# Kernel tuning notes

Hardware: AMD Instinct MI355X
Metric: run time of the kernel (lower is better)

## Reference

```python
import jax, jax.numpy as jnp
import numpy as np

N_NODES = 100000
N_EDGES = 1200000
IN_DIM = 64
OUT_DIM = 64
LN_EPS = 1e-5


def setup_inputs() -> dict:
    key = jax.random.key(0)
    k_x, k_e, k_w, k_b, k_g, k_beta = jax.random.split(key, 6)
    x = jax.random.normal(k_x, (N_NODES, IN_DIM), dtype=jnp.float32)
    edge_index = jax.random.randint(k_e, (2, N_EDGES), 0, N_NODES, dtype=jnp.int64)
    # nn.Linear(in_dim*2, out_dim): weight [out, 2*in], bias [out]
    lim = 1.0 / np.sqrt(2 * IN_DIM)
    W = jax.random.uniform(k_w, (OUT_DIM, 2 * IN_DIM), minval=-lim, maxval=lim, dtype=jnp.float32)
    b = jax.random.uniform(k_b, (OUT_DIM,), minval=-lim, maxval=lim, dtype=jnp.float32)
    gamma = jnp.ones((OUT_DIM,), dtype=jnp.float32)
    beta = jnp.zeros((OUT_DIM,), dtype=jnp.float32)
    return {"x": x, "W": W, "b": b, "gamma": gamma, "beta": beta, "edge_index": edge_index}


def reference(x, W, b, gamma, beta, edge_index):
    i = edge_index[0]  # destination nodes (aggregation target)
    j = edge_index[1]  # source nodes (neighbor features)
    n = x.shape[0]
    # mean aggregation: scatter-add gathered neighbor feats, divide by degree
    agg = jax.ops.segment_sum(x[j], i, num_segments=n)  # [N, in_dim]
    deg = jax.ops.segment_sum(jnp.ones(i.shape, x.dtype), i, num_segments=n)
    agg = agg / jnp.maximum(deg, 1.0)[:, None]
    # concat + linear + relu
    h = jnp.concatenate([x, agg], axis=-1) @ W.T + b  # [N, out_dim]
    h = jax.nn.relu(h)
    # layernorm (dropout p=0 is identity in eval)
    mu = jnp.mean(h, axis=-1, keepdims=True)
    var = jnp.var(h, axis=-1, keepdims=True)
    return (h - mu) / jnp.sqrt(var + LN_EPS) * gamma + beta
```

## Files before the change

kernel.cpp:

```cpp
#include <hip/hip_runtime.h>
#include <hip/hip_bf16.h>

#define N_NODES 100000
#define N_EDGES 1200000
#define LN_EPS 1e-5f
#define CAP 40
#define NBIN 782
#define NREP 8
#define BCAPR 288
#define EPB 4096
#define P1_BLOCKS 293
#define CONV_BLOCKS 507
#define NSTRIDE 42
#define NBLK2 1563
#define QENC (127.0f / 5.2f)
#define QDEC (5.2f / 127.0f)

typedef __attribute__((ext_vector_type(8))) short short8;
typedef __attribute__((ext_vector_type(8))) unsigned short us8;
typedef __attribute__((ext_vector_type(4))) float float4v;
typedef __attribute__((ext_vector_type(2))) int   ivec2;

__device__ __forceinline__ short bfb(float v) {
    __hip_bfloat16 h = __float2bfloat16(v);
    short s; __builtin_memcpy(&s, &h, 2); return s;
}
__device__ __forceinline__ int q8(float v) {
    return (int)rintf(fminf(fmaxf(v * QENC, -127.0f), 127.0f));
}

__global__ __launch_bounds__(256) void k_bin3(
    const float* __restrict__ x, unsigned short* __restrict__ xb,
    char* __restrict__ xq,
    const float* __restrict__ W, unsigned short* __restrict__ Wb,
    const int* __restrict__ ei, int* __restrict__ btail,
    int* __restrict__ binbuf)
{
    const int tid = threadIdx.x;

    if (blockIdx.x >= P1_BLOCKS) {
        if (blockIdx.x == P1_BLOCKS) {
            if (tid < 8) {
                short8 z = {0, 0, 0, 0, 0, 0, 0, 0};
                *(short8*)(xb + (size_t)N_NODES * 64 + tid * 8) = z;
                *(ivec2*)(xq + (size_t)N_NODES * 64 + tid * 8) = (ivec2){0, 0};
            }
#pragma unroll
            for (int it = 0; it < 32; ++it) {
                int i = it * 256 + tid;
                Wb[i] = (unsigned short)bfb(W[i]);
            }
        }
        for (int i = (blockIdx.x - P1_BLOCKS) * 256 + tid; i < N_NODES * 8;
             i += CONV_BLOCKS * 256) {
            float4v f0 = *(const float4v*)(x + 8 * i);
            float4v f1 = *(const float4v*)(x + 8 * i + 4);
            short8 p;
            p[0] = bfb(f0.x); p[1] = bfb(f0.y); p[2] = bfb(f0.z); p[3] = bfb(f0.w);
            p[4] = bfb(f1.x); p[5] = bfb(f1.y); p[6] = bfb(f1.z); p[7] = bfb(f1.w);
            *(short8*)(xb + 8 * i) = p;
            int w0 = (q8(f0.x) & 255) | ((q8(f0.y) & 255) << 8) |
                     ((q8(f0.z) & 255) << 16) | ((q8(f0.w) & 255) << 24);
            int w1 = (q8(f1.x) & 255) | ((q8(f1.y) & 255) << 8) |
                     ((q8(f1.z) & 255) << 16) | ((q8(f1.w) & 255) << 24);
            *(ivec2*)(xq + 8 * (size_t)i) = (ivec2){w0, w1};
        }
        return;
    }

    __shared__ int   bcnt[NBIN];
    __shared__ int   bbase[NBIN];
    __shared__ int   bgbase[NBIN];
    __shared__ int   bfill[NBIN];
    __shared__ int   scanbuf[256];
    __shared__ ivec2 stage[EPB];

    const int rep = blockIdx.x & (NREP - 1);

    for (int i = tid; i < NBIN; i += 256) { bcnt[i] = 0; bfill[i] = 0; }
    __syncthreads();

    const int ebase = blockIdx.x * EPB;
    int d[16], s[16];
#pragma unroll
    for (int u = 0; u < 16; ++u) {
        int e = ebase + u * 256 + tid;
        bool v = (e < N_EDGES);
        d[u] = v ? ei[e] : -1;
        s[u] = v ? ei[N_EDGES + e] : 0;
        if (v) atomicAdd(&bcnt[d[u] >> 7], 1);
    }
    __syncthreads();

    int v4[4], tsum = 0;
#pragma unroll
    for (int k = 0; k < 4; ++k) {
        int b = 4 * tid + k;
        v4[k] = (b < NBIN) ? bcnt[b] : 0;
        tsum += v4[k];
    }
    scanbuf[tid] = tsum;
    __syncthreads();
    for (int off = 1; off < 256; off <<= 1) {
        int t = (tid >= off) ? scanbuf[tid - off] : 0;
        __syncthreads();
        scanbuf[tid] += t;
        __syncthreads();
    }
    int run = scanbuf[tid] - tsum;
#pragma unroll
    for (int k = 0; k < 4; ++k) {
        int b = 4 * tid + k;
        if (b < NBIN) bbase[b] = run;
        run += v4[k];
    }
    const int tot = scanbuf[255];

    for (int b = tid; b < NBIN; b += 256) {
        int c = bcnt[b];
        bgbase[b] = c ? atomicAdd(&btail[rep * NBIN + b], c) : 0;
    }
    __syncthreads();

#pragma unroll
    for (int u = 0; u < 16; ++u) {
        if (d[u] >= 0) {
            int b = d[u] >> 7;
            int p = bbase[b] + atomicAdd(&bfill[b], 1);
            stage[p] = (ivec2){d[u], s[u]};
        }
    }
    __syncthreads();

    for (int i = tid; i < tot; i += 256) {
        ivec2 e = stage[i];
        int b = e.x >> 7;
        int pos = bgbase[b] + (i - bbase[b]);
        if (pos < BCAPR)
            binbuf[((size_t)rep * NBIN + b) * BCAPR + pos] = ((e.x & 127) << 17) | e.y;
    }
}

__global__ __launch_bounds__(256, 4) void node_fused(
    const unsigned short* __restrict__ xb, const char* __restrict__ xq,
    const unsigned short* __restrict__ Wb,
    const int* __restrict__ btail, const int* __restrict__ binbuf,
    const float* __restrict__ bias,
    const float* __restrict__ gamma, const float* __restrict__ beta,
    float* __restrict__ out)
{
    __shared__ short Wl[64 * 136];
    __shared__ int   nlist[64 * NSTRIDE];
    __shared__ int   lcnt[64];

    const int tid = threadIdx.x;
    const int bin  = blockIdx.x >> 1;
    const int half = blockIdx.x & 1;
    const int nodebase = blockIdx.x * 64;

#pragma unroll
    for (int it = 0; it < 4; ++it) {
        int i = it * 256 + tid;
        int row = i >> 4, c8 = i & 15;
        *(short8*)&Wl[row * 136 + c8 * 8] = *(const short8*)(Wb + row * 128 + c8 * 8);
    }
    if (tid < 64) lcnt[tid] = 0;
    __syncthreads();

#pragma unroll
    for (int rep = 0; rep < NREP; ++rep) {
        const int nb = min(btail[rep * NBIN + bin], BCAPR);
        const int* bp = binbuf + ((size_t)rep * NBIN + bin) * BCAPR;
        for (int i = tid; i < nb; i += 256) {
            int pk = bp[i];
            int nl = (pk >> 17) - (half << 6);
            if ((unsigned)nl < 64u) {
                int slot = atomicAdd(&lcnt[nl], 1);
                if (slot < CAP) nlist[nl * NSTRIDE + slot] = pk & 0x1FFFF;
            }
        }
    }
    __syncthreads();

    const int wid  = tid >> 6;
    const int lane = tid & 63;
    const int g    = lane >> 4;
    const int c    = lane & 15;
    const int ch   = c & 7;
    const int pr   = c >> 3;
    const int nbase = nodebase + wid * 16;
    if (nbase >= N_NODES) return;

    int dfull[4], dgs[4];
#pragma unroll
    for (int r = 0; r < 4; ++r) {
        dfull[r] = lcnt[wid * 16 + r * 4 + g];
        dgs[r]   = min(dfull[r], CAP);
    }
    int aai[4][8];
#pragma unroll
    for (int r = 0; r < 4; ++r)
#pragma unroll
        for (int k = 0; k < 8; ++k) aai[r][k] = 0;

    const int dmax = max(max(dgs[0], dgs[1]), max(dgs[2], dgs[3]));
    for (int t = 0; t < dmax; t += 16) {
        ivec2 vv[32];
#pragma unroll
        for (int u = 0; u < 8; ++u)
#pragma unroll
            for (int r = 0; r < 4; ++r) {
                int idx = t + 2 * u + pr;
                int wl  = nlist[(wid * 16 + r * 4 + g) * NSTRIDE + idx];
                int j   = (idx < dgs[r]) ? wl : N_NODES;
                vv[u * 4 + r] = *(const ivec2*)(xq + (size_t)j * 64 + ch * 8);
            }
#pragma unroll
        for (int u = 0; u < 8; ++u)
#pragma unroll
            for (int r = 0; r < 4; ++r) {
                int w0 = vv[u * 4 + r].x, w1 = vv[u * 4 + r].y;
                aai[r][0] += (w0 << 24) >> 24;
                aai[r][1] += (w0 << 16) >> 24;
                aai[r][2] += (w0 << 8)  >> 24;
                aai[r][3] +=  w0 >> 24;
                aai[r][4] += (w1 << 24) >> 24;
                aai[r][5] += (w1 << 16) >> 24;
                aai[r][6] += (w1 << 8)  >> 24;
                aai[r][7] +=  w1 >> 24;
            }
    }

    const unsigned short* xrow = xb + (size_t)(nbase + c) * 64 + g * 8;
    short8 A0 = *(const short8*)(xrow);
    short8 A1 = *(const short8*)(xrow + 32);

#pragma unroll
    for (int r = 0; r < 4; ++r)
#pragma unroll
        for (int k = 0; k < 8; ++k) aai[r][k] += __shfl_xor(aai[r][k], 8);

    short* aL = (short*)&nlist[wid * 16 * NSTRIDE];
#pragma unroll
    for (int r = 0; r < 4; ++r) {
        float rd = QDEC / fmaxf((float)dfull[r], 1.0f);
        int m = r * 4 + g;
        short8 p;
#pragma unroll
        for (int k = 0; k < 8; ++k) p[k] = bfb((float)aai[r][k] * rd);
        if (pr == 0)
            *(short8*)(aL + m * 72 + ch * 8) = p;
    }
    short8 A2 = *(const short8*)(aL + c * 72 + g * 8);
    short8 A3 = *(const short8*)(aL + c * 72 + 32 + g * 8);

    float bs_[4], gm_[4], bt_[4];
#pragma unroll
    for (int ct = 0; ct < 4; ++ct) {
        bs_[ct] = bias[ct * 16 + c];
        gm_[ct] = gamma[ct * 16 + c];
        bt_[ct] = beta[ct * 16 + c];
    }

    float4v acc[4];
#pragma unroll
    for (int ct = 0; ct < 4; ++ct) {
        float bb = bs_[ct];
        acc[ct] = (float4v){bb, bb, bb, bb};
    }
#pragma unroll
    for (int ks = 0; ks < 4; ++ks) {
        short8 Af = (ks == 0) ? A0 : (ks == 1) ? A1 : (ks == 2) ? A2 : A3;
#pragma unroll
        for (int ct = 0; ct < 4; ++ct) {
            short8 Bf = *(const short8*)(Wl + (ct * 16 + c) * 136 + ks * 32 + g * 8);
            acc[ct] = __builtin_amdgcn_mfma_f32_16x16x32_bf16(Af, Bf, acc[ct], 0, 0, 0);
        }
    }

    float s_[4] = {0, 0, 0, 0}, q_[4] = {0, 0, 0, 0};
#pragma unroll
    for (int ct = 0; ct < 4; ++ct)
#pragma unroll
        for (int r = 0; r < 4; ++r) {
            float h = fmaxf(acc[ct][r], 0.0f);
            acc[ct][r] = h;
            s_[r] += h;
            q_[r] += h * h;
        }
#pragma unroll
    for (int off = 1; off <= 8; off <<= 1)
#pragma unroll
        for (int r = 0; r < 4; ++r) {
            s_[r] += __shfl_xor(s_[r], off);
            q_[r] += __shfl_xor(q_[r], off);
        }
#pragma unroll
    for (int r = 0; r < 4; ++r) {
        float mu = s_[r] * (1.0f / 64.0f);
        float var = q_[r] * (1.0f / 64.0f) - mu * mu;
        float is = rsqrtf(var + LN_EPS);
        int node = nbase + g * 4 + r;
        if (node < N_NODES) {
#pragma unroll
            for (int ct = 0; ct < 4; ++ct) {
                out[node * 64 + ct * 16 + c] =
                    (acc[ct][r] - mu) * is * gm_[ct] + bt_[ct];
            }
        }
    }
}

extern "C" void kernel_launch(void* const* d_in, const int* in_sizes, int n_in,
                              void* d_out, int out_size, void* d_ws, size_t ws_size,
                              hipStream_t stream) {
    const float* x     = (const float*)d_in[0];
    const float* W     = (const float*)d_in[1];
    const float* b     = (const float*)d_in[2];
    const float* gamma = (const float*)d_in[3];
    const float* beta  = (const float*)d_in[4];
    const int*   ei    = (const int*)d_in[5];
    float* out = (float*)d_out;

    int* btail = (int*)d_ws;
    int* binbuf = (int*)((char*)d_ws + 32768);
    unsigned short* xb = (unsigned short*)(binbuf + (size_t)NREP * NBIN * BCAPR);
    unsigned short* Wb = xb + (size_t)(N_NODES + 1) * 64;
    char* xq = (char*)(Wb + 8192);

    (void)hipMemsetAsync(btail, 0, NREP * NBIN * sizeof(int), stream);

    k_bin3<<<P1_BLOCKS + CONV_BLOCKS, 256, 0, stream>>>(x, xb, xq, W, Wb, ei, btail, binbuf);
    node_fused<<<NBLK2, 256, 0, stream>>>(xb, xq, Wb, btail, binbuf, b, gamma, beta, out);
}
```

Measured before the change: 134.6 us.

## Aggregate neighbor features via LDS atomics per 128-node bin

Replaces the per-node neighbor-list build followed by register accumulation with an edge-parallel scheme. Each block processes a whole 128-node bin, gathers the quantized source rows and adds them into a shared int accumulator with LDS atomics, then runs the MFMA and layernorm epilogue on two 16-node groups per wave. The goal is to remove the degree cap and the load imbalance from padding to the max degree across nodes, and to halve the block count. The cost is many LDS atomic adds (eight per edge per channel group), W read from global instead of LDS, and a larger shared-memory footprint.

```diff
diff --git a/kernel.cpp b/kernel.cpp
--- a/kernel.cpp
+++ b/kernel.cpp
@@ -4,20 +4,16 @@
 #define N_NODES 100000
 #define N_EDGES 1200000
 #define LN_EPS 1e-5f
-#define CAP 40
 #define NBIN 782
 #define NREP 8
 #define BCAPR 288
 #define EPB 4096
 #define P1_BLOCKS 293
 #define CONV_BLOCKS 507
-#define NSTRIDE 42
-#define NBLK2 1563
 #define QENC (127.0f / 5.2f)
 #define QDEC (5.2f / 127.0f)
 
 typedef __attribute__((ext_vector_type(8))) short short8;
-typedef __attribute__((ext_vector_type(8))) unsigned short us8;
 typedef __attribute__((ext_vector_type(4))) float float4v;
 typedef __attribute__((ext_vector_type(2))) int   ivec2;
 
@@ -149,35 +145,59 @@
     const float* __restrict__ gamma, const float* __restrict__ beta,
     float* __restrict__ out)
 {
-    __shared__ short Wl[64 * 136];
-    __shared__ int   nlist[64 * NSTRIDE];
-    __shared__ int   lcnt[64];
+    __shared__ int agg[129][66];
+    __shared__ int deg[132];
 
     const int tid = threadIdx.x;
-    const int bin  = blockIdx.x >> 1;
-    const int half = blockIdx.x & 1;
-    const int nodebase = blockIdx.x * 64;
-
-#pragma unroll
-    for (int it = 0; it < 4; ++it) {
-        int i = it * 256 + tid;
-        int row = i >> 4, c8 = i & 15;
-        *(short8*)&Wl[row * 136 + c8 * 8] = *(const short8*)(Wb + row * 128 + c8 * 8);
-    }
-    if (tid < 64) lcnt[tid] = 0;
-    __syncthreads();
-
-#pragma unroll
-    for (int rep = 0; rep < NREP; ++rep) {
-        const int nb = min(btail[rep * NBIN + bin], BCAPR);
-        const int* bp = binbuf + ((size_t)rep * NBIN + bin) * BCAPR;
-        for (int i = tid; i < nb; i += 256) {
-            int pk = bp[i];
-            int nl = (pk >> 17) - (half << 6);
-            if ((unsigned)nl < 64u) {
-                int slot = atomicAdd(&lcnt[nl], 1);
-                if (slot < CAP) nlist[nl * NSTRIDE + slot] = pk & 0x1FFFF;
-            }
+    const int bin = blockIdx.x;
+
+    for (int i = tid; i < 129 * 66; i += 256) ((int*)agg)[i] = 0;
+    if (tid < 132) deg[tid] = 0;
+    __syncthreads();
+
+    int cum[NREP + 1];
+    cum[0] = 0;
+#pragma unroll
+    for (int r2 = 0; r2 < NREP; ++r2)
+        cum[r2 + 1] = cum[r2] + min(btail[r2 * NBIN + bin], BCAPR);
+    const int etot = cum[NREP];
+
+    const int eo = tid >> 3;
+    const int ch = tid & 7;
+
+    for (int base = 0; base < etot; base += 512) {
+        int pk[16];
+#pragma unroll
+        for (int u = 0; u < 16; ++u) {
+            int v = base + u * 32 + eo;
+            int rp = 0;
+#pragma unroll
+            for (int k2 = 1; k2 < NREP; ++k2) rp += (v >= cum[k2]);
+            int idx = v - cum[rp];
+            pk[u] = (v < etot)
+                  ? binbuf[((size_t)rp * NBIN + bin) * BCAPR + idx]
+                  : ((128 << 17) | N_NODES);
+        }
+        ivec2 vv[16];
+#pragma unroll
+        for (int u = 0; u < 16; ++u) {
+            int j = pk[u] & 0x1FFFF;
+            vv[u] = *(const ivec2*)(xq + (size_t)j * 64 + ch * 8);
+        }
+#pragma unroll
+        for (int u = 0; u < 16; ++u) {
+            int nl = pk[u] >> 17;
+            int w0 = vv[u].x, w1 = vv[u].y;
+            int* ap = &agg[nl][ch * 8];
+            atomicAdd(ap + 0, (w0 << 24) >> 24);
+            atomicAdd(ap + 1, (w0 << 16) >> 24);
+            atomicAdd(ap + 2, (w0 << 8)  >> 24);
+            atomicAdd(ap + 3,  w0 >> 24);
+            atomicAdd(ap + 4, (w1 << 24) >> 24);
+            atomicAdd(ap + 5, (w1 << 16) >> 24);
+            atomicAdd(ap + 6, (w1 << 8)  >> 24);
+            atomicAdd(ap + 7,  w1 >> 24);
+            if (ch == 0) atomicAdd(&deg[nl], 1);
         }
     }
     __syncthreads();
@@ -186,73 +206,6 @@
     const int lane = tid & 63;
     const int g    = lane >> 4;
     const int c    = lane & 15;
-    const int ch   = c & 7;
-    const int pr   = c >> 3;
-    const int nbase = nodebase + wid * 16;
-    if (nbase >= N_NODES) return;
-
-    int dfull[4], dgs[4];
-#pragma unroll
-    for (int r = 0; r < 4; ++r) {
-        dfull[r] = lcnt[wid * 16 + r * 4 + g];
-        dgs[r]   = min(dfull[r], CAP);
-    }
-    int aai[4][8];
-#pragma unroll
-    for (int r = 0; r < 4; ++r)
-#pragma unroll
-        for (int k = 0; k < 8; ++k) aai[r][k] = 0;
-
-    const int dmax = max(max(dgs[0], dgs[1]), max(dgs[2], dgs[3]));
-    for (int t = 0; t < dmax; t += 16) {
-        ivec2 vv[32];
-#pragma unroll
-        for (int u = 0; u < 8; ++u)
-#pragma unroll
-            for (int r = 0; r < 4; ++r) {
-                int idx = t + 2 * u + pr;
-                int wl  = nlist[(wid * 16 + r * 4 + g) * NSTRIDE + idx];
-                int j   = (idx < dgs[r]) ? wl : N_NODES;
-                vv[u * 4 + r] = *(const ivec2*)(xq + (size_t)j * 64 + ch * 8);
-            }
-#pragma unroll
-        for (int u = 0; u < 8; ++u)
-#pragma unroll
-            for (int r = 0; r < 4; ++r) {
-                int w0 = vv[u * 4 + r].x, w1 = vv[u * 4 + r].y;
-                aai[r][0] += (w0 << 24) >> 24;
-                aai[r][1] += (w0 << 16) >> 24;
-                aai[r][2] += (w0 << 8)  >> 24;
-                aai[r][3] +=  w0 >> 24;
-                aai[r][4] += (w1 << 24) >> 24;
-                aai[r][5] += (w1 << 16) >> 24;
-                aai[r][6] += (w1 << 8)  >> 24;
-                aai[r][7] +=  w1 >> 24;
-            }
-    }
-
-    const unsigned short* xrow = xb + (size_t)(nbase + c) * 64 + g * 8;
-    short8 A0 = *(const short8*)(xrow);
-    short8 A1 = *(const short8*)(xrow + 32);
-
-#pragma unroll
-    for (int r = 0; r < 4; ++r)
-#pragma unroll
-        for (int k = 0; k < 8; ++k) aai[r][k] += __shfl_xor(aai[r][k], 8);
-
-    short* aL = (short*)&nlist[wid * 16 * NSTRIDE];
-#pragma unroll
-    for (int r = 0; r < 4; ++r) {
-        float rd = QDEC / fmaxf((float)dfull[r], 1.0f);
-        int m = r * 4 + g;
-        short8 p;
-#pragma unroll
-        for (int k = 0; k < 8; ++k) p[k] = bfb((float)aai[r][k] * rd);
-        if (pr == 0)
-            *(short8*)(aL + m * 72 + ch * 8) = p;
-    }
-    short8 A2 = *(const short8*)(aL + c * 72 + g * 8);
-    short8 A3 = *(const short8*)(aL + c * 72 + 32 + g * 8);
 
     float bs_[4], gm_[4], bt_[4];
 #pragma unroll
@@ -262,50 +215,68 @@
         bt_[ct] = beta[ct * 16 + c];
     }
 
-    float4v acc[4];
-#pragma unroll
-    for (int ct = 0; ct < 4; ++ct) {
-        float bb = bs_[ct];
-        acc[ct] = (float4v){bb, bb, bb, bb};
-    }
-#pragma unroll
-    for (int ks = 0; ks < 4; ++ks) {
-        short8 Af = (ks == 0) ? A0 : (ks == 1) ? A1 : (ks == 2) ? A2 : A3;
+    for (int gi = 0; gi < 2; ++gi) {
+        const int nbase = bin * 128 + wid * 32 + gi * 16;
+        if (nbase >= N_NODES) break;
+
+        const unsigned short* xrow = xb + (size_t)(nbase + c) * 64 + g * 8;
+        short8 A0 = *(const short8*)(xrow);
+        short8 A1 = *(const short8*)(xrow + 32);
+
+        const int nloc = wid * 32 + gi * 16 + c;
+        const float rd = QDEC / fmaxf((float)deg[nloc], 1.0f);
+        short8 A2, A3;
+#pragma unroll
+        for (int k2 = 0; k2 < 8; ++k2) {
+            A2[k2] = bfb((float)agg[nloc][g * 8 + k2] * rd);
+            A3[k2] = bfb((float)agg[nloc][32 + g * 8 + k2] * rd);
+        }
+
+        float4v acc[4];
 #pragma unroll
         for (int ct = 0; ct < 4; ++ct) {
-            short8 Bf = *(const short8*)(Wl + (ct * 16 + c) * 136 + ks * 32 + g * 8);
-            acc[ct] = __builtin_amdgcn_mfma_f32_16x16x32_bf16(Af, Bf, acc[ct], 0, 0, 0);
-        }
-    }
-
-    float s_[4] = {0, 0, 0, 0}, q_[4] = {0, 0, 0, 0};
-#pragma unroll
-    for (int ct = 0; ct < 4; ++ct)
+            float bb = bs_[ct];
+            acc[ct] = (float4v){bb, bb, bb, bb};
+        }
+#pragma unroll
+        for (int ks = 0; ks < 4; ++ks) {
+            short8 Af = (ks == 0) ? A0 : (ks == 1) ? A1 : (ks == 2) ? A2 : A3;
+#pragma unroll
+            for (int ct = 0; ct < 4; ++ct) {
+                short8 Bf = *(const short8*)(Wb + (ct * 16 + c) * 128 + ks * 32 + g * 8);
+                acc[ct] = __builtin_amdgcn_mfma_f32_16x16x32_bf16(Af, Bf, acc[ct], 0, 0, 0);
+            }
+        }
+
+        float s_[4] = {0, 0, 0, 0}, q_[4] = {0, 0, 0, 0};
+#pragma unroll
+        for (int ct = 0; ct < 4; ++ct)
+#pragma unroll
+            for (int r = 0; r < 4; ++r) {
+                float h = fmaxf(acc[ct][r], 0.0f);
+                acc[ct][r] = h;
+                s_[r] += h;
+                q_[r] += h * h;
+            }
+#pragma unroll
+        for (int off = 1; off <= 8; off <<= 1)
+#pragma unroll
+            for (int r = 0; r < 4; ++r) {
+                s_[r] += __shfl_xor(s_[r], off);
+                q_[r] += __shfl_xor(q_[r], off);
+            }
 #pragma unroll
         for (int r = 0; r < 4; ++r) {
-            float h = fmaxf(acc[ct][r], 0.0f);
-            acc[ct][r] = h;
-            s_[r] += h;
-            q_[r] += h * h;
-        }
-#pragma unroll
-    for (int off = 1; off <= 8; off <<= 1)
-#pragma unroll
-        for (int r = 0; r < 4; ++r) {
-            s_[r] += __shfl_xor(s_[r], off);
-            q_[r] += __shfl_xor(q_[r], off);
-        }
-#pragma unroll
-    for (int r = 0; r < 4; ++r) {
-        float mu = s_[r] * (1.0f / 64.0f);
-        float var = q_[r] * (1.0f / 64.0f) - mu * mu;
-        float is = rsqrtf(var + LN_EPS);
-        int node = nbase + g * 4 + r;
-        if (node < N_NODES) {
-#pragma unroll
-            for (int ct = 0; ct < 4; ++ct) {
-                out[node * 64 + ct * 16 + c] =
-                    (acc[ct][r] - mu) * is * gm_[ct] + bt_[ct];
+            float mu = s_[r] * (1.0f / 64.0f);
+            float var = q_[r] * (1.0f / 64.0f) - mu * mu;
+            float is = rsqrtf(var + LN_EPS);
+            int node = nbase + g * 4 + r;
+            if (node < N_NODES) {
+#pragma unroll
+                for (int ct = 0; ct < 4; ++ct) {
+                    out[node * 64 + ct * 16 + c] =
+                        (acc[ct][r] - mu) * is * gm_[ct] + bt_[ct];
+                }
             }
         }
     }
@@ -331,5 +302,5 @@
     (void)hipMemsetAsync(btail, 0, NREP * NBIN * sizeof(int), stream);
 
     k_bin3<<<P1_BLOCKS + CONV_BLOCKS, 256, 0, stream>>>(x, xb, xq, W, Wb, ei, btail, binbuf);
-    node_fused<<<NBLK2, 256, 0, stream>>>(xb, xq, Wb, btail, binbuf, b, gamma, beta, out);
-}
+    node_fused<<<NBIN, 256, 0, stream>>>(xb, xq, Wb, btail, binbuf, b, gamma, beta, out);
+}
```

New measurement: 157.2 us. 16.8% more time.

## Drop bf16 copy of x, read fp32 directly; double edges per binning block

Applied to the files above, without the earlier changes.

Removes the intermediate bf16 copy of x: node_fused now reads fp32 rows of x directly and converts them to bf16 in registers. This drops one full write of x and the matching read of the bf16 buffer. The binning kernel now handles 8192 edges per block with half as many blocks, re-reading edge indices in the second pass instead of holding them in registers. Its LDS stage array is split into a packed int plus a 16-bit bin id. In exchange, node_fused reads twice as many bytes for its own rows, and the binning phase has fewer blocks and reads ei twice.

```diff
diff --git a/kernel.cpp b/kernel.cpp
--- a/kernel.cpp
+++ b/kernel.cpp
@@ -8,8 +8,8 @@
 #define NBIN 782
 #define NREP 8
 #define BCAPR 288
-#define EPB 4096
-#define P1_BLOCKS 293
+#define EPB 8192
+#define P1_BLOCKS 147
 #define CONV_BLOCKS 507
 #define NSTRIDE 42
 #define NBLK2 1563
@@ -17,7 +17,6 @@
 #define QDEC (5.2f / 127.0f)
 
 typedef __attribute__((ext_vector_type(8))) short short8;
-typedef __attribute__((ext_vector_type(8))) unsigned short us8;
 typedef __attribute__((ext_vector_type(4))) float float4v;
 typedef __attribute__((ext_vector_type(2))) int   ivec2;
 
@@ -30,8 +29,7 @@
 }
 
 __global__ __launch_bounds__(256) void k_bin3(
-    const float* __restrict__ x, unsigned short* __restrict__ xb,
-    char* __restrict__ xq,
+    const float* __restrict__ x, char* __restrict__ xq,
     const float* __restrict__ W, unsigned short* __restrict__ Wb,
     const int* __restrict__ ei, int* __restrict__ btail,
     int* __restrict__ binbuf)
@@ -40,11 +38,8 @@
 
     if (blockIdx.x >= P1_BLOCKS) {
         if (blockIdx.x == P1_BLOCKS) {
-            if (tid < 8) {
-                short8 z = {0, 0, 0, 0, 0, 0, 0, 0};
-                *(short8*)(xb + (size_t)N_NODES * 64 + tid * 8) = z;
+            if (tid < 8)
                 *(ivec2*)(xq + (size_t)N_NODES * 64 + tid * 8) = (ivec2){0, 0};
-            }
 #pragma unroll
             for (int it = 0; it < 32; ++it) {
                 int i = it * 256 + tid;
@@ -55,10 +50,6 @@
              i += CONV_BLOCKS * 256) {
             float4v f0 = *(const float4v*)(x + 8 * i);
             float4v f1 = *(const float4v*)(x + 8 * i + 4);
-            short8 p;
-            p[0] = bfb(f0.x); p[1] = bfb(f0.y); p[2] = bfb(f0.z); p[3] = bfb(f0.w);
-            p[4] = bfb(f1.x); p[5] = bfb(f1.y); p[6] = bfb(f1.z); p[7] = bfb(f1.w);
-            *(short8*)(xb + 8 * i) = p;
             int w0 = (q8(f0.x) & 255) | ((q8(f0.y) & 255) << 8) |
                      ((q8(f0.z) & 255) << 16) | ((q8(f0.w) & 255) << 24);
             int w1 = (q8(f1.x) & 255) | ((q8(f1.y) & 255) << 8) |
@@ -73,7 +64,8 @@
     __shared__ int   bgbase[NBIN];
     __shared__ int   bfill[NBIN];
     __shared__ int   scanbuf[256];
-    __shared__ ivec2 stage[EPB];
+    __shared__ int   stage[EPB];
+    __shared__ unsigned short stgb[EPB];
 
     const int rep = blockIdx.x & (NREP - 1);
 
@@ -81,14 +73,10 @@
     __syncthreads();
 
     const int ebase = blockIdx.x * EPB;
-    int d[16], s[16];
-#pragma unroll
-    for (int u = 0; u < 16; ++u) {
+#pragma unroll
+    for (int u = 0; u < 32; ++u) {
         int e = ebase + u * 256 + tid;
-        bool v = (e < N_EDGES);
-        d[u] = v ? ei[e] : -1;
-        s[u] = v ? ei[N_EDGES + e] : 0;
-        if (v) atomicAdd(&bcnt[d[u] >> 7], 1);
+        if (e < N_EDGES) atomicAdd(&bcnt[ei[e] >> 7], 1);
     }
     __syncthreads();
 
@@ -123,26 +111,28 @@
     __syncthreads();
 
 #pragma unroll
-    for (int u = 0; u < 16; ++u) {
-        if (d[u] >= 0) {
-            int b = d[u] >> 7;
+    for (int u = 0; u < 32; ++u) {
+        int e = ebase + u * 256 + tid;
+        if (e < N_EDGES) {
+            int d = ei[e], s = ei[N_EDGES + e];
+            int b = d >> 7;
             int p = bbase[b] + atomicAdd(&bfill[b], 1);
-            stage[p] = (ivec2){d[u], s[u]};
+            stage[p] = ((d & 127) << 17) | s;
+            stgb[p]  = (unsigned short)b;
         }
     }
     __syncthreads();
 
     for (int i = tid; i < tot; i += 256) {
-        ivec2 e = stage[i];
-        int b = e.x >> 7;
+        int b = stgb[i];
         int pos = bgbase[b] + (i - bbase[b]);
         if (pos < BCAPR)
-            binbuf[((size_t)rep * NBIN + b) * BCAPR + pos] = ((e.x & 127) << 17) | e.y;
+            binbuf[((size_t)rep * NBIN + b) * BCAPR + pos] = stage[i];
     }
 }
 
 __global__ __launch_bounds__(256, 4) void node_fused(
-    const unsigned short* __restrict__ xb, const char* __restrict__ xq,
+    const float* __restrict__ x, const char* __restrict__ xq,
     const unsigned short* __restrict__ Wb,
     const int* __restrict__ btail, const int* __restrict__ binbuf,
     const float* __restrict__ bias,
@@ -231,9 +221,16 @@
             }
     }
 
-    const unsigned short* xrow = xb + (size_t)(nbase + c) * 64 + g * 8;
-    short8 A0 = *(const short8*)(xrow);
-    short8 A1 = *(const short8*)(xrow + 32);
+    const float* xr = x + (size_t)(nbase + c) * 64 + g * 8;
+    float4v f0 = *(const float4v*)(xr);
+    float4v f1 = *(const float4v*)(xr + 4);
+    float4v f2 = *(const float4v*)(xr + 32);
+    float4v f3 = *(const float4v*)(xr + 36);
+    short8 A0, A1;
+    A0[0] = bfb(f0.x); A0[1] = bfb(f0.y); A0[2] = bfb(f0.z); A0[3] = bfb(f0.w);
+    A0[4] = bfb(f1.x); A0[5] = bfb(f1.y); A0[6] = bfb(f1.z); A0[7] = bfb(f1.w);
+    A1[0] = bfb(f2.x); A1[1] = bfb(f2.y); A1[2] = bfb(f2.z); A1[3] = bfb(f2.w);
+    A1[4] = bfb(f3.x); A1[5] = bfb(f3.y); A1[6] = bfb(f3.z); A1[7] = bfb(f3.w);
 
 #pragma unroll
     for (int r = 0; r < 4; ++r)
@@ -324,12 +321,11 @@
 
     int* btail = (int*)d_ws;
     int* binbuf = (int*)((char*)d_ws + 32768);
-    unsigned short* xb = (unsigned short*)(binbuf + (size_t)NREP * NBIN * BCAPR);
-    unsigned short* Wb = xb + (size_t)(N_NODES + 1) * 64;
+    unsigned short* Wb = (unsigned short*)(binbuf + (size_t)NREP * NBIN * BCAPR);
     char* xq = (char*)(Wb + 8192);
 
     (void)hipMemsetAsync(btail, 0, NREP * NBIN * sizeof(int), stream);
 
-    k_bin3<<<P1_BLOCKS + CONV_BLOCKS, 256, 0, stream>>>(x, xb, xq, W, Wb, ei, btail, binbuf);
-    node_fused<<<NBLK2, 256, 0, stream>>>(xb, xq, Wb, btail, binbuf, b, gamma, beta, out);
-}
+    k_bin3<<<P1_BLOCKS + CONV_BLOCKS, 256, 0, stream>>>(x, xq, W, Wb, ei, btail, binbuf);
+    node_fused<<<NBLK2, 256, 0, stream>>>(x, xq, Wb, btail, binbuf, b, gamma, beta, out);
+}
```

After: 148.0 us. 9.9% more time.
